# Performance work log

Measured on AMD Instinct MI355X. Metric: run time of the kernel, lower is better.

The kernel has to match this reference:

```python
import jax, jax.numpy as jnp
import numpy as np

N = 65536          # nodes
E = 1048576        # edges
IN_C = 128
HID_C = 32
HEADS = 4
OUT_C = 64
NEG_SLOPE = 0.2
EPS = 1e-16


def gat_conv(x, edge_index, W, att_src, att_dst, bias, heads, out_c, concat):
    """PyG-style GATConv. x: [N, F_in]; edge_index: [2, E] (row=src, col=dst).
    W: [F_in, heads*out_c]; att_src/att_dst: [heads, out_c]; bias: [heads*out_c] or [out_c]."""
    src, dst = edge_index[0], edge_index[1]
    n = x.shape[0]
    h = (x @ W).reshape(n, heads, out_c)                      # [N, H, C]
    a_src = jnp.einsum('nhc,hc->nh', h, att_src)              # [N, H]
    a_dst = jnp.einsum('nhc,hc->nh', h, att_dst)              # [N, H]
    alpha = a_src[src] + a_dst[dst]                           # [E, H]
    alpha = jax.nn.leaky_relu(alpha, NEG_SLOPE)
    # segment softmax over incoming edges of each destination node
    amax = jax.ops.segment_max(alpha, dst, num_segments=n)    # [N, H]
    alpha = jnp.exp(alpha - amax[dst])
    denom = jax.ops.segment_sum(alpha, dst, num_segments=n)   # [N, H]
    alpha = alpha / (denom[dst] + EPS)
    # weighted scatter-add aggregation
    msgs = alpha[:, :, None] * h[src]                         # [E, H, C]
    out = jax.ops.segment_sum(msgs, dst, num_segments=n)      # [N, H, C]
    if concat:
        out = out.reshape(n, heads * out_c)
    else:
        out = out.mean(axis=1)
    return out + bias


def setup_inputs() -> dict:
    key = jax.random.key(0)
    ks = jax.random.split(key, 10)
    s_in = 1.0 / np.sqrt(IN_C)
    s_h = 1.0 / np.sqrt(HEADS * HID_C)
    x = jax.random.normal(ks[0], (N, IN_C), dtype=jnp.float32)
    edge_index = jax.random.randint(ks[1], (2, E), 0, N, dtype=jnp.int64)
    W1 = jax.random.normal(ks[2], (IN_C, HEADS * HID_C), dtype=jnp.float32) * s_in
    att_src1 = jax.random.normal(ks[3], (HEADS, HID_C), dtype=jnp.float32) * s_h
    att_dst1 = jax.random.normal(ks[4], (HEADS, HID_C), dtype=jnp.float32) * s_h
    b1 = jnp.zeros((HEADS * HID_C,), dtype=jnp.float32)
    W2 = jax.random.normal(ks[5], (HEADS * HID_C, OUT_C), dtype=jnp.float32) * s_h
    att_src2 = jax.random.normal(ks[6], (1, OUT_C), dtype=jnp.float32) * s_h
    att_dst2 = jax.random.normal(ks[7], (1, OUT_C), dtype=jnp.float32) * s_h
    b2 = jnp.zeros((OUT_C,), dtype=jnp.float32)
    return {"x": x, "edge_index": edge_index, "W1": W1, "att_src1": att_src1,
            "att_dst1": att_dst1, "b1": b1, "W2": W2, "att_src2": att_src2,
            "att_dst2": att_dst2, "b2": b2}


def reference(x, edge_index, W1, att_src1, att_dst1, b1, W2, att_src2, att_dst2, b2):
    # dropout is identity in eval mode
    h = gat_conv(x, edge_index, W1, att_src1, att_dst1, b1, HEADS, HID_C, concat=True)
    h = jax.nn.sigmoid(h)
    h = gat_conv(h, edge_index, W2, att_src2, att_dst2, b2, 1, OUT_C, concat=True)
    return jax.nn.sigmoid(h)
```

## Files before the change

kernel.cpp:

```cpp
#include <hip/hip_runtime.h>
#include <hip/hip_fp16.h>

#define N_NODES 65536
#define N_EDGES 1048576
#define NBUCK 256
#define PBLOCKS 256
#define EPB (N_EDGES / PBLOCKS)
#define K4CAP 6144
constexpr float NEG = 0.2f;
constexpr float EPS_ = 1e-16f;
constexpr float WSHIFT = 2.7725887f;

typedef __attribute__((ext_vector_type(8))) short bf16x8;
typedef __attribute__((ext_vector_type(4))) float f32x4;

__device__ __forceinline__ unsigned short f2bf(float f) {
    unsigned int u = __float_as_uint(f);
    return (unsigned short)((u + 0x7fffu + ((u >> 16) & 1u)) >> 16);
}
__device__ __forceinline__ unsigned short f2h(float f) {
    __half_raw r = __half_raw(__float2half(f));
    return r.x;
}
__device__ __forceinline__ __half2 u2h2(unsigned int u) {
    union { unsigned int u; __half2 h; } c; c.u = u; return c.h;
}
__device__ __forceinline__ unsigned int h22u(__half2 h) {
    union { unsigned int u; __half2 h; } c; c.h = h; return c.u;
}
__device__ __forceinline__ float lrelu_exp_s(float l) {
    return __expf(fmaxf(l, NEG * l) - WSHIFT);
}


__global__ __launch_bounds__(256) void coarse_hist(const int* __restrict__ ei,
                                                   int* __restrict__ hist_mat) {
    __shared__ int h[NBUCK];
    int t = threadIdx.x;
    h[t] = 0;
    __syncthreads();
    int base = blockIdx.x * EPB;
    #pragma unroll
    for (int i = 0; i < EPB / 256; ++i) {
        int d = ei[N_EDGES + base + i * 256 + t];
        atomicAdd(&h[d >> 8], 1);
    }
    __syncthreads();
    hist_mat[t * PBLOCKS + blockIdx.x] = h[t];
}

__global__ __launch_bounds__(1024) void scan_a(const int* __restrict__ in,
                                               int* __restrict__ out,
                                               int* __restrict__ bsum) {
    __shared__ int sm[1024];
    int t = threadIdx.x, i = blockIdx.x * 1024 + t;
    int v = in[i];
    sm[t] = v;
    __syncthreads();
    for (int off = 1; off < 1024; off <<= 1) {
        int u = (t >= off) ? sm[t - off] : 0;
        __syncthreads();
        sm[t] += u;
        __syncthreads();
    }
    out[i] = sm[t] - v;
    if (t == 1023) bsum[blockIdx.x] = sm[t];
}

__global__ __launch_bounds__(1024) void scan_c(int* __restrict__ arr,
                                               const int* __restrict__ bsum) {
    __shared__ int off[64];
    int t = threadIdx.x;
    if (t < 64) {
        int v = bsum[t];
        int incl = v;
        #pragma unroll
        for (int o = 1; o < 64; o <<= 1) {
            int u = __shfl_up(incl, o);
            if (t >= o) incl += u;
        }
        off[t] = incl - v;
    }
    __syncthreads();
    int i = blockIdx.x * 1024 + t;
    arr[i] += off[blockIdx.x];
}

__global__ __launch_bounds__(256) void partition_kernel(const int* __restrict__ ei,
                                                        const int* __restrict__ cursor_mat,
                                                        unsigned int* __restrict__ edge_part) {
    __shared__ int h[NBUCK];
    __shared__ int start[NBUCK];
    __shared__ int cur[NBUCK];
    __shared__ int gcur[NBUCK];
    __shared__ unsigned int stage[EPB];
    int t = threadIdx.x;
    h[t] = 0;
    gcur[t] = cursor_mat[t * PBLOCKS + blockIdx.x];
    __syncthreads();
    unsigned int ent[EPB / 256];
    int base = blockIdx.x * EPB;
    #pragma unroll
    for (int i = 0; i < EPB / 256; ++i) {
        int e = base + i * 256 + t;
        int s = ei[e], d = ei[N_EDGES + e];
        ent[i] = ((unsigned int)s << 16) | (unsigned int)d;
        atomicAdd(&h[d >> 8], 1);
    }
    __syncthreads();
    int v = h[t];
    start[t] = v;
    __syncthreads();
    for (int off = 1; off < 256; off <<= 1) {
        int u = (t >= off) ? start[t - off] : 0;
        __syncthreads();
        start[t] += u;
        __syncthreads();
    }
    int excl = start[t] - v;
    start[t] = excl;
    cur[t] = excl;
    __syncthreads();
    #pragma unroll
    for (int i = 0; i < EPB / 256; ++i) {
        int b = (int)((ent[i] & 0xffffu) >> 8);
        int slot = atomicAdd(&cur[b], 1);
        stage[slot] = ent[i];
    }
    __syncthreads();
    int s0 = t * (EPB / 256);
    #pragma unroll
    for (int i = 0; i < EPB / 256; ++i) {
        unsigned int p = stage[s0 + i];
        int b = (int)((p & 0xffffu) >> 8);
        edge_part[gcur[b] + (s0 + i - start[b])] = p;
    }
}

__global__ __launch_bounds__(256) void finalize_kernel(const unsigned int* __restrict__ edge_part,
                                                       const int* __restrict__ cursor_mat,
                                                       int* __restrict__ row_ptr,
                                                       int* __restrict__ csr_src) {
    __shared__ int h[256];
    __shared__ int sc[256];
    __shared__ int cur[256];
    __shared__ unsigned short stage[K4CAP];
    int t = threadIdx.x;
    int b = blockIdx.x;
    if (b == NBUCK - 1 && t == 0) row_ptr[N_NODES] = N_EDGES;
    int cs = cursor_mat[b * PBLOCKS];
    int ce = (b == NBUCK - 1) ? N_EDGES : cursor_mat[(b + 1) * PBLOCKS];
    int cnt = ce - cs;
    h[t] = 0;
    __syncthreads();
    for (int i = t; i < cnt; i += 256)
        atomicAdd(&h[edge_part[cs + i] & 0xffu], 1);
    __syncthreads();
    int v = h[t];
    sc[t] = v;
    __syncthreads();
    for (int off = 1; off < 256; off <<= 1) {
        int u = (t >= off) ? sc[t - off] : 0;
        __syncthreads();
        sc[t] += u;
        __syncthreads();
    }
    int excl = sc[t] - v;
    row_ptr[b * 256 + t] = cs + excl;
    cur[t] = excl;
    __syncthreads();
    if (cnt <= K4CAP) {
        for (int i = t; i < cnt; i += 256) {
            unsigned int p = edge_part[cs + i];
            int slot = atomicAdd(&cur[p & 0xffu], 1);
            stage[slot] = (unsigned short)(p >> 16);
        }
        __syncthreads();
        for (int i = t; i < cnt; i += 256)
            csr_src[cs + i] = (int)stage[i];
    } else {
        for (int i = t; i < cnt; i += 256) {
            unsigned int p = edge_part[cs + i];
            int slot = atomicAdd(&cur[p & 0xffu], 1);
            csr_src[cs + slot] = (int)(p >> 16);
        }
    }
}


template <int OUTC>
__global__ __launch_bounds__(256) void gemm_mfma(const float* __restrict__ X,
                                                 const float* __restrict__ W,
                                                 unsigned short* __restrict__ H) {
    constexpr int NT = OUTC / 16;
    extern __shared__ unsigned short Wl[];
    int t = threadIdx.x;
    for (int idx = t; idx < OUTC * 128; idx += 256) {
        int j = idx & 7;
        int ln = (idx >> 3) & 63;
        int fc = idx >> 9;
        int kc = fc & 3, ct = fc >> 2;
        int k = kc * 32 + (ln >> 4) * 8 + j;
        int n = ct * 16 + (ln & 15);
        Wl[idx] = (unsigned short)f2bf(W[k * OUTC + n]);
    }
    __syncthreads();
    int wave = t >> 6, lane = t & 63;
    int m = lane & 15, quad = lane >> 4;
    int node_base = blockIdx.x * 64 + wave * 16;
    const float* xrow = X + (size_t)(node_base + m) * 128 + quad * 8;
    bf16x8 a[4];
    #pragma unroll
    for (int kc = 0; kc < 4; ++kc) {
        float4 u = *(const float4*)(xrow + kc * 32);
        float4 v = *(const float4*)(xrow + kc * 32 + 4);
        bf16x8 af;
        af[0] = (short)f2bf(u.x); af[1] = (short)f2bf(u.y);
        af[2] = (short)f2bf(u.z); af[3] = (short)f2bf(u.w);
        af[4] = (short)f2bf(v.x); af[5] = (short)f2bf(v.y);
        af[6] = (short)f2bf(v.z); af[7] = (short)f2bf(v.w);
        a[kc] = af;
    }
    #pragma unroll
    for (int ct = 0; ct < NT; ++ct) {
        f32x4 acc = {0.f, 0.f, 0.f, 0.f};
        #pragma unroll
        for (int kc = 0; kc < 4; ++kc) {
            bf16x8 bfr = *(const bf16x8*)(Wl + ((ct * 4 + kc) * 64 + lane) * 8);
            acc = __builtin_amdgcn_mfma_f32_16x16x32_bf16(a[kc], bfr, acc, 0, 0, 0);
        }
        #pragma unroll
        for (int r = 0; r < 4; ++r) {
            int row = quad * 4 + r;
            H[(size_t)(node_base + row) * OUTC + ct * 16 + m] = f2h(acc[r]);
        }
    }
}


__global__ __launch_bounds__(256) void att1_kernel(const unsigned int* __restrict__ h1u,
                                                   const float* __restrict__ as_w,
                                                   const float* __restrict__ ad_w,
                                                   float* __restrict__ a_src,
                                                   float* __restrict__ a_dst) {
    int wave = (blockIdx.x * 256 + threadIdx.x) >> 6;
    int lane = threadIdx.x & 63;
    __half2 p = u2h2(h1u[wave * 64 + lane]);
    float h0 = __low2float(p), h1v = __high2float(p);
    float2 sw = *(const float2*)(as_w + lane * 2);
    float2 dw = *(const float2*)(ad_w + lane * 2);
    float ps = h0 * sw.x + h1v * sw.y;
    float pd = h0 * dw.x + h1v * dw.y;
    #pragma unroll
    for (int m = 1; m < 16; m <<= 1) {
        ps += __shfl_xor(ps, m);
        pd += __shfl_xor(pd, m);
    }
    if ((lane & 15) == 0) {
        a_src[wave * 4 + (lane >> 4)] = ps;
        a_dst[wave * 4 + (lane >> 4)] = pd;
    }
}

__global__ __launch_bounds__(256) void att2_kernel(const __half* __restrict__ h2h,
                                                   const float* __restrict__ as_w,
                                                   const float* __restrict__ ad_w,
                                                   float* __restrict__ a_src,
                                                   float* __restrict__ a_dst) {
    int wave = (blockIdx.x * 256 + threadIdx.x) >> 6;
    int lane = threadIdx.x & 63;
    float v = __half2float(h2h[wave * 64 + lane]);
    float ps = v * as_w[lane];
    float pd = v * ad_w[lane];
    #pragma unroll
    for (int m = 1; m < 64; m <<= 1) {
        ps += __shfl_xor(ps, m);
        pd += __shfl_xor(pd, m);
    }
    if (lane == 0) {
        a_src[wave] = ps;
        a_dst[wave] = pd;
    }
}


__global__ __launch_bounds__(256) void agg1_kernel(const int* __restrict__ row_ptr,
                                                   const int* __restrict__ csr_src,
                                                   const unsigned int* __restrict__ h1u,
                                                   const float* __restrict__ a_src,
                                                   const float* __restrict__ a_dst,
                                                   const float* __restrict__ b1,
                                                   float* __restrict__ x2) {
    int n = (blockIdx.x * 256 + threadIdx.x) >> 6;
    int lane = threadIdx.x & 63;
    int quad = lane >> 4;
    int col = lane & 15;
    int j16 = lane & 15;
    int hd_c = col >> 2;
    int src_base = hd_c * 16 + quad;
    float adw = a_dst[n * 4 + quad];
    int e = row_ptr[n], end = row_ptr[n + 1];
    __half2 acc0 = u2h2(0u), acc1 = u2h2(0u), acc2 = u2h2(0u), acc3 = u2h2(0u);
    float denom = 0.f;
    while (e < end) {
        int mb = end - e;
        if (mb > 16) mb = 16;
        int s_l = csr_src[e + (j16 < mb ? j16 : 0)];
        float l = a_src[s_l * 4 + quad] + adw;
        float wv = (j16 < mb) ? lrelu_exp_s(l) : 0.f;
        denom += wv;
        unsigned int pack = ((unsigned int)f2h(wv) << 16) | (unsigned int)s_l;
        #pragma unroll
        for (int g = 0; g < 4; ++g) {
            unsigned int pk = __shfl(pack, src_base + g * 4);
            unsigned int wu = pk >> 16;
            __half2 w2 = u2h2(wu | (wu << 16));
            unsigned int s = pk & 0xffffu;
            uint4 hv = *(const uint4*)(h1u + s * 64 + col * 4);
            acc0 = __hfma2(w2, u2h2(hv.x), acc0);
            acc1 = __hfma2(w2, u2h2(hv.y), acc1);
            acc2 = __hfma2(w2, u2h2(hv.z), acc2);
            acc3 = __hfma2(w2, u2h2(hv.w), acc3);
        }
        e += 16;
    }
    #pragma unroll
    for (int m = 16; m < 64; m <<= 1) {
        acc0 = __hadd2(acc0, u2h2(__shfl_xor(h22u(acc0), m)));
        acc1 = __hadd2(acc1, u2h2(__shfl_xor(h22u(acc1), m)));
        acc2 = __hadd2(acc2, u2h2(__shfl_xor(h22u(acc2), m)));
        acc3 = __hadd2(acc3, u2h2(__shfl_xor(h22u(acc3), m)));
    }
    #pragma unroll
    for (int m = 1; m < 16; m <<= 1) denom += __shfl_xor(denom, m);
    float dfin = __shfl(denom, hd_c * 16);
    if (quad == 0) {
        float inv = 1.f / (dfin + EPS_);
        int c0 = col * 8;
        float v[8];
        v[0] = __low2float(acc0); v[1] = __high2float(acc0);
        v[2] = __low2float(acc1); v[3] = __high2float(acc1);
        v[4] = __low2float(acc2); v[5] = __high2float(acc2);
        v[6] = __low2float(acc3); v[7] = __high2float(acc3);
        float o[8];
        #pragma unroll
        for (int i = 0; i < 8; ++i) {
            float u = v[i] * inv + b1[c0 + i];
            o[i] = 1.f / (1.f + __expf(-u));
        }
        float4* dst = (float4*)(x2 + (size_t)n * 128 + c0);
        dst[0] = make_float4(o[0], o[1], o[2], o[3]);
        dst[1] = make_float4(o[4], o[5], o[6], o[7]);
    }
}


__global__ __launch_bounds__(256) void agg2_kernel(const int* __restrict__ row_ptr,
                                                   const int* __restrict__ csr_src,
                                                   const unsigned int* __restrict__ h2u,
                                                   const float* __restrict__ a_src,
                                                   const float* __restrict__ a_dst,
                                                   const float* __restrict__ b2,
                                                   float* __restrict__ out) {
    int n = (blockIdx.x * 256 + threadIdx.x) >> 6;
    int lane = threadIdx.x & 63;
    int grp = lane >> 3;
    int col = lane & 7;
    int j16 = lane & 15;
    float ad = a_dst[n];
    int e = row_ptr[n], end = row_ptr[n + 1];
    __half2 acc0 = u2h2(0u), acc1 = u2h2(0u), acc2 = u2h2(0u), acc3 = u2h2(0u);
    float denom = 0.f;
    while (e < end) {
        int mb = end - e;
        if (mb > 16) mb = 16;
        int s_l = csr_src[e + (j16 < mb ? j16 : 0)];
        float l = a_src[s_l] + ad;
        float wv = (j16 < mb) ? lrelu_exp_s(l) : 0.f;
        denom += wv;
        unsigned int pack = ((unsigned int)f2h(wv) << 16) | (unsigned int)s_l;
        #pragma unroll
        for (int g = 0; g < 2; ++g) {
            unsigned int pk = __shfl(pack, g * 8 + grp);
            unsigned int wu = pk >> 16;
            __half2 w2 = u2h2(wu | (wu << 16));
            unsigned int s = pk & 0xffffu;
            uint4 hv = *(const uint4*)(h2u + s * 32 + col * 4);
            acc0 = __hfma2(w2, u2h2(hv.x), acc0);
            acc1 = __hfma2(w2, u2h2(hv.y), acc1);
            acc2 = __hfma2(w2, u2h2(hv.z), acc2);
            acc3 = __hfma2(w2, u2h2(hv.w), acc3);
        }
        e += 16;
    }
    #pragma unroll
    for (int m = 8; m < 64; m <<= 1) {
        acc0 = __hadd2(acc0, u2h2(__shfl_xor(h22u(acc0), m)));
        acc1 = __hadd2(acc1, u2h2(__shfl_xor(h22u(acc1), m)));
        acc2 = __hadd2(acc2, u2h2(__shfl_xor(h22u(acc2), m)));
        acc3 = __hadd2(acc3, u2h2(__shfl_xor(h22u(acc3), m)));
    }
    #pragma unroll
    for (int m = 1; m < 16; m <<= 1) denom += __shfl_xor(denom, m);
    if (lane < 8) {
        float inv = 1.f / (denom + EPS_);
        int c0 = col * 8;
        float v[8];
        v[0] = __low2float(acc0); v[1] = __high2float(acc0);
        v[2] = __low2float(acc1); v[3] = __high2float(acc1);
        v[4] = __low2float(acc2); v[5] = __high2float(acc2);
        v[6] = __low2float(acc3); v[7] = __high2float(acc3);
        float o[8];
        #pragma unroll
        for (int i = 0; i < 8; ++i) {
            float u = v[i] * inv + b2[c0 + i];
            o[i] = 1.f / (1.f + __expf(-u));
        }
        float4* dst = (float4*)(out + (size_t)n * 64 + c0);
        dst[0] = make_float4(o[0], o[1], o[2], o[3]);
        dst[1] = make_float4(o[4], o[5], o[6], o[7]);
    }
}


extern "C" void kernel_launch(void* const* d_in, const int* in_sizes, int n_in,
                              void* d_out, int out_size, void* d_ws, size_t ws_size,
                              hipStream_t stream) {
    (void)in_sizes; (void)n_in; (void)out_size; (void)ws_size;
    const float* x   = (const float*)d_in[0];
    const int*   ei  = (const int*)d_in[1];
    const float* W1  = (const float*)d_in[2];
    const float* as1 = (const float*)d_in[3];
    const float* ad1 = (const float*)d_in[4];
    const float* b1  = (const float*)d_in[5];
    const float* W2  = (const float*)d_in[6];
    const float* as2 = (const float*)d_in[7];
    const float* ad2 = (const float*)d_in[8];
    const float* b2  = (const float*)d_in[9];
    float* out = (float*)d_out;

    char* p = (char*)d_ws;
    auto alloc = [&](size_t bytes) -> void* {
        void* r = (void*)p;
        p += (bytes + 255) & ~(size_t)255;
        return r;
    };
    int* hist_mat   = (int*)alloc((size_t)NBUCK * PBLOCKS * 4);
    int* cursor_mat = (int*)alloc((size_t)NBUCK * PBLOCKS * 4);
    int* bsum       = (int*)alloc(64 * 4);
    unsigned int* edge_part = (unsigned int*)alloc((size_t)N_EDGES * 4);
    int* row_ptr    = (int*)alloc((size_t)(N_NODES + 1) * 4);
    int* csr_src    = (int*)alloc((size_t)N_EDGES * 4);
    unsigned short* h1 = (unsigned short*)alloc((size_t)N_NODES * 128 * 2);
    float* a_src1   = (float*)alloc((size_t)N_NODES * 4 * 4);
    float* a_dst1   = (float*)alloc((size_t)N_NODES * 4 * 4);
    float* x2       = (float*)alloc((size_t)N_NODES * 128 * 4);
    unsigned short* h2 = (unsigned short*)alloc((size_t)N_NODES * 64 * 2);
    float* a_src2   = (float*)alloc((size_t)N_NODES * 4);
    float* a_dst2   = (float*)alloc((size_t)N_NODES * 4);

    coarse_hist<<<PBLOCKS, 256, 0, stream>>>(ei, hist_mat);
    scan_a<<<64, 1024, 0, stream>>>(hist_mat, cursor_mat, bsum);
    scan_c<<<64, 1024, 0, stream>>>(cursor_mat, bsum);
    partition_kernel<<<PBLOCKS, 256, 0, stream>>>(ei, cursor_mat, edge_part);
    finalize_kernel<<<NBUCK, 256, 0, stream>>>(edge_part, cursor_mat, row_ptr, csr_src);

    gemm_mfma<128><<<N_NODES / 64, 256, 128 * 128 * 2, stream>>>(x, W1, h1);
    att1_kernel<<<N_NODES / 4, 256, 0, stream>>>((const unsigned int*)h1, as1, ad1, a_src1, a_dst1);
    agg1_kernel<<<N_NODES / 4, 256, 0, stream>>>(row_ptr, csr_src, (const unsigned int*)h1,
                                                 a_src1, a_dst1, b1, x2);

    gemm_mfma<64><<<N_NODES / 64, 256, 128 * 64 * 2, stream>>>(x2, W2, h2);
    att2_kernel<<<N_NODES / 4, 256, 0, stream>>>((const __half*)h2, as2, ad2, a_src2, a_dst2);
    agg2_kernel<<<N_NODES / 4, 256, 0, stream>>>(row_ptr, csr_src, (const unsigned int*)h2,
                                                 a_src2, a_dst2, b2, out);
}
```

Measured before the change: 258.4 us.

## Process two nodes per wave in aggregation and store layer-1 output as bf16

The aggregation kernels now map two destination nodes onto each 64-lane wave, 32 lanes per node, with 8-edge chunks instead of 16. This cuts lane waste for the average in-degree of about 16 and shortens the cross-lane reductions. Layer-1 output x2 is now written as bf16 instead of fp32, halving its write and read traffic. gemm2 is specialised to load bf16 directly, removing its conversion step. The cost is more loop iterations per node and a small precision loss in the hidden activations.

New measurement: 249.0 us. 1.04x faster.

```diff
diff --git a/kernel.cpp b/kernel.cpp
--- a/kernel.cpp
+++ b/kernel.cpp
@@ -188,10 +188,10 @@
 }
 
 
-template <int OUTC>
-__global__ __launch_bounds__(256) void gemm_mfma(const float* __restrict__ X,
-                                                 const float* __restrict__ W,
-                                                 unsigned short* __restrict__ H) {
+__global__ __launch_bounds__(256) void gemm1_mfma(const float* __restrict__ X,
+                                                  const float* __restrict__ W,
+                                                  unsigned short* __restrict__ H) {
+    constexpr int OUTC = 128;
     constexpr int NT = OUTC / 16;
     extern __shared__ unsigned short Wl[];
     int t = threadIdx.x;
@@ -221,6 +221,47 @@
         af[6] = (short)f2bf(v.z); af[7] = (short)f2bf(v.w);
         a[kc] = af;
     }
+    #pragma unroll
+    for (int ct = 0; ct < NT; ++ct) {
+        f32x4 acc = {0.f, 0.f, 0.f, 0.f};
+        #pragma unroll
+        for (int kc = 0; kc < 4; ++kc) {
+            bf16x8 bfr = *(const bf16x8*)(Wl + ((ct * 4 + kc) * 64 + lane) * 8);
+            acc = __builtin_amdgcn_mfma_f32_16x16x32_bf16(a[kc], bfr, acc, 0, 0, 0);
+        }
+        #pragma unroll
+        for (int r = 0; r < 4; ++r) {
+            int row = quad * 4 + r;
+            H[(size_t)(node_base + row) * OUTC + ct * 16 + m] = f2h(acc[r]);
+        }
+    }
+}
+
+
+__global__ __launch_bounds__(256) void gemm2_mfma(const unsigned short* __restrict__ X,
+                                                  const float* __restrict__ W,
+                                                  unsigned short* __restrict__ H) {
+    constexpr int OUTC = 64;
+    constexpr int NT = OUTC / 16;
+    extern __shared__ unsigned short Wl[];
+    int t = threadIdx.x;
+    for (int idx = t; idx < OUTC * 128; idx += 256) {
+        int j = idx & 7;
+        int ln = (idx >> 3) & 63;
+        int fc = idx >> 9;
+        int kc = fc & 3, ct = fc >> 2;
+        int k = kc * 32 + (ln >> 4) * 8 + j;
+        int n = ct * 16 + (ln & 15);
+        Wl[idx] = (unsigned short)f2bf(W[k * OUTC + n]);
+    }
+    __syncthreads();
+    int wave = t >> 6, lane = t & 63;
+    int m = lane & 15, quad = lane >> 4;
+    int node_base = blockIdx.x * 64 + wave * 16;
+    const unsigned short* xrow = X + (size_t)(node_base + m) * 128 + quad * 8;
+    bf16x8 a[4];
+    #pragma unroll
+    for (int kc = 0; kc < 4; ++kc) a[kc] = *(const bf16x8*)(xrow + kc * 32);
     #pragma unroll
     for (int ct = 0; ct < NT; ++ct) {
         f32x4 acc = {0.f, 0.f, 0.f, 0.f};
@@ -290,29 +331,33 @@
                                                    const float* __restrict__ a_src,
                                                    const float* __restrict__ a_dst,
                                                    const float* __restrict__ b1,
-                                                   float* __restrict__ x2) {
-    int n = (blockIdx.x * 256 + threadIdx.x) >> 6;
+                                                   unsigned short* __restrict__ x2) {
+    int wave = (blockIdx.x * 256 + threadIdx.x) >> 6;
     int lane = threadIdx.x & 63;
-    int quad = lane >> 4;
-    int col = lane & 15;
-    int j16 = lane & 15;
+    int half = lane >> 5;
+    int ln = lane & 31;
+    int n = wave * 2 + half;
+    int j8 = ln & 7;
+    int whead = ln >> 3;
+    int sub = ln >> 4;
+    int col = ln & 15;
     int hd_c = col >> 2;
-    int src_base = hd_c * 16 + quad;
-    float adw = a_dst[n * 4 + quad];
+    int rbase = half * 32 + hd_c * 8 + sub;
+    float adw = a_dst[n * 4 + whead];
     int e = row_ptr[n], end = row_ptr[n + 1];
     __half2 acc0 = u2h2(0u), acc1 = u2h2(0u), acc2 = u2h2(0u), acc3 = u2h2(0u);
     float denom = 0.f;
     while (e < end) {
         int mb = end - e;
-        if (mb > 16) mb = 16;
-        int s_l = csr_src[e + (j16 < mb ? j16 : 0)];
-        float l = a_src[s_l * 4 + quad] + adw;
-        float wv = (j16 < mb) ? lrelu_exp_s(l) : 0.f;
+        if (mb > 8) mb = 8;
+        int s_l = csr_src[e + (j8 < mb ? j8 : 0)];
+        float l = a_src[s_l * 4 + whead] + adw;
+        float wv = (j8 < mb) ? lrelu_exp_s(l) : 0.f;
         denom += wv;
         unsigned int pack = ((unsigned int)f2h(wv) << 16) | (unsigned int)s_l;
         #pragma unroll
         for (int g = 0; g < 4; ++g) {
-            unsigned int pk = __shfl(pack, src_base + g * 4);
+            unsigned int pk = __shfl(pack, rbase + g * 2);
             unsigned int wu = pk >> 16;
             __half2 w2 = u2h2(wu | (wu << 16));
             unsigned int s = pk & 0xffffu;
@@ -322,19 +367,16 @@
             acc2 = __hfma2(w2, u2h2(hv.z), acc2);
             acc3 = __hfma2(w2, u2h2(hv.w), acc3);
         }
-        e += 16;
-    }
-    #pragma unroll
-    for (int m = 16; m < 64; m <<= 1) {
-        acc0 = __hadd2(acc0, u2h2(__shfl_xor(h22u(acc0), m)));
-        acc1 = __hadd2(acc1, u2h2(__shfl_xor(h22u(acc1), m)));
-        acc2 = __hadd2(acc2, u2h2(__shfl_xor(h22u(acc2), m)));
-        acc3 = __hadd2(acc3, u2h2(__shfl_xor(h22u(acc3), m)));
-    }
-    #pragma unroll
-    for (int m = 1; m < 16; m <<= 1) denom += __shfl_xor(denom, m);
-    float dfin = __shfl(denom, hd_c * 16);
-    if (quad == 0) {
+        e += 8;
+    }
+    acc0 = __hadd2(acc0, u2h2(__shfl_xor(h22u(acc0), 16)));
+    acc1 = __hadd2(acc1, u2h2(__shfl_xor(h22u(acc1), 16)));
+    acc2 = __hadd2(acc2, u2h2(__shfl_xor(h22u(acc2), 16)));
+    acc3 = __hadd2(acc3, u2h2(__shfl_xor(h22u(acc3), 16)));
+    #pragma unroll
+    for (int m = 1; m < 8; m <<= 1) denom += __shfl_xor(denom, m);
+    float dfin = __shfl(denom, half * 32 + hd_c * 8);
+    if (sub == 0) {
         float inv = 1.f / (dfin + EPS_);
         int c0 = col * 8;
         float v[8];
@@ -342,15 +384,16 @@
         v[2] = __low2float(acc1); v[3] = __high2float(acc1);
         v[4] = __low2float(acc2); v[5] = __high2float(acc2);
         v[6] = __low2float(acc3); v[7] = __high2float(acc3);
-        float o[8];
-        #pragma unroll
-        for (int i = 0; i < 8; ++i) {
-            float u = v[i] * inv + b1[c0 + i];
-            o[i] = 1.f / (1.f + __expf(-u));
-        }
-        float4* dst = (float4*)(x2 + (size_t)n * 128 + c0);
-        dst[0] = make_float4(o[0], o[1], o[2], o[3]);
-        dst[1] = make_float4(o[4], o[5], o[6], o[7]);
+        unsigned int o[4];
+        #pragma unroll
+        for (int i = 0; i < 4; ++i) {
+            float u0 = v[2 * i] * inv + b1[c0 + 2 * i];
+            float u1 = v[2 * i + 1] * inv + b1[c0 + 2 * i + 1];
+            u0 = 1.f / (1.f + __expf(-u0));
+            u1 = 1.f / (1.f + __expf(-u1));
+            o[i] = (unsigned int)f2bf(u0) | ((unsigned int)f2bf(u1) << 16);
+        }
+        *(uint4*)(x2 + (size_t)n * 128 + c0) = make_uint4(o[0], o[1], o[2], o[3]);
     }
 }
 
@@ -362,26 +405,30 @@
                                                    const float* __restrict__ a_dst,
                                                    const float* __restrict__ b2,
                                                    float* __restrict__ out) {
-    int n = (blockIdx.x * 256 + threadIdx.x) >> 6;
+    int wave = (blockIdx.x * 256 + threadIdx.x) >> 6;
     int lane = threadIdx.x & 63;
-    int grp = lane >> 3;
-    int col = lane & 7;
-    int j16 = lane & 15;
+    int half = lane >> 5;
+    int ln = lane & 31;
+    int n = wave * 2 + half;
+    int j8 = ln & 7;
+    int sub = (ln >> 3) & 3;
+    int col = ln & 7;
+    int rbase = half * 32 + sub;
     float ad = a_dst[n];
     int e = row_ptr[n], end = row_ptr[n + 1];
     __half2 acc0 = u2h2(0u), acc1 = u2h2(0u), acc2 = u2h2(0u), acc3 = u2h2(0u);
     float denom = 0.f;
     while (e < end) {
         int mb = end - e;
-        if (mb > 16) mb = 16;
-        int s_l = csr_src[e + (j16 < mb ? j16 : 0)];
+        if (mb > 8) mb = 8;
+        int s_l = csr_src[e + (j8 < mb ? j8 : 0)];
         float l = a_src[s_l] + ad;
-        float wv = (j16 < mb) ? lrelu_exp_s(l) : 0.f;
+        float wv = (j8 < mb) ? lrelu_exp_s(l) : 0.f;
         denom += wv;
         unsigned int pack = ((unsigned int)f2h(wv) << 16) | (unsigned int)s_l;
         #pragma unroll
         for (int g = 0; g < 2; ++g) {
-            unsigned int pk = __shfl(pack, g * 8 + grp);
+            unsigned int pk = __shfl(pack, rbase + g * 4);
             unsigned int wu = pk >> 16;
             __half2 w2 = u2h2(wu | (wu << 16));
             unsigned int s = pk & 0xffffu;
@@ -391,18 +438,18 @@
             acc2 = __hfma2(w2, u2h2(hv.z), acc2);
             acc3 = __hfma2(w2, u2h2(hv.w), acc3);
         }
-        e += 16;
-    }
-    #pragma unroll
-    for (int m = 8; m < 64; m <<= 1) {
+        e += 8;
+    }
+    #pragma unroll
+    for (int m = 8; m < 32; m <<= 1) {
         acc0 = __hadd2(acc0, u2h2(__shfl_xor(h22u(acc0), m)));
         acc1 = __hadd2(acc1, u2h2(__shfl_xor(h22u(acc1), m)));
         acc2 = __hadd2(acc2, u2h2(__shfl_xor(h22u(acc2), m)));
         acc3 = __hadd2(acc3, u2h2(__shfl_xor(h22u(acc3), m)));
     }
     #pragma unroll
-    for (int m = 1; m < 16; m <<= 1) denom += __shfl_xor(denom, m);
-    if (lane < 8) {
+    for (int m = 1; m < 8; m <<= 1) denom += __shfl_xor(denom, m);
+    if (sub == 0) {
         float inv = 1.f / (denom + EPS_);
         int c0 = col * 8;
         float v[8];
@@ -454,7 +501,7 @@
     unsigned short* h1 = (unsigned short*)alloc((size_t)N_NODES * 128 * 2);
     float* a_src1   = (float*)alloc((size_t)N_NODES * 4 * 4);
     float* a_dst1   = (float*)alloc((size_t)N_NODES * 4 * 4);
-    float* x2       = (float*)alloc((size_t)N_NODES * 128 * 4);
+    unsigned short* x2 = (unsigned short*)alloc((size_t)N_NODES * 128 * 2);
     unsigned short* h2 = (unsigned short*)alloc((size_t)N_NODES * 64 * 2);
     float* a_src2   = (float*)alloc((size_t)N_NODES * 4);
     float* a_dst2   = (float*)alloc((size_t)N_NODES * 4);
@@ -465,13 +512,13 @@
     partition_kernel<<<PBLOCKS, 256, 0, stream>>>(ei, cursor_mat, edge_part);
     finalize_kernel<<<NBUCK, 256, 0, stream>>>(edge_part, cursor_mat, row_ptr, csr_src);
 
-    gemm_mfma<128><<<N_NODES / 64, 256, 128 * 128 * 2, stream>>>(x, W1, h1);
+    gemm1_mfma<<<N_NODES / 64, 256, 128 * 128 * 2, stream>>>(x, W1, h1);
     att1_kernel<<<N_NODES / 4, 256, 0, stream>>>((const unsigned int*)h1, as1, ad1, a_src1, a_dst1);
-    agg1_kernel<<<N_NODES / 4, 256, 0, stream>>>(row_ptr, csr_src, (const unsigned int*)h1,
+    agg1_kernel<<<N_NODES / 8, 256, 0, stream>>>(row_ptr, csr_src, (const unsigned int*)h1,
                                                  a_src1, a_dst1, b1, x2);
 
-    gemm_mfma<64><<<N_NODES / 64, 256, 128 * 64 * 2, stream>>>(x2, W2, h2);
+    gemm2_mfma<<<N_NODES / 64, 256, 128 * 64 * 2, stream>>>(x2, W2, h2);
     att2_kernel<<<N_NODES / 4, 256, 0, stream>>>((const __half*)h2, as2, ad2, a_src2, a_dst2);
-    agg2_kernel<<<N_NODES / 4, 256, 0, stream>>>(row_ptr, csr_src, (const unsigned int*)h2,
+    agg2_kernel<<<N_NODES / 8, 256, 0, stream>>>(row_ptr, csr_src, (const unsigned int*)h2,
                                                  a_src2, a_dst2, b2, out);
 }
```
